# Optimization experiments

Hardware: AMD Instinct MI355X
Metric: run time of the kernel (lower is better)

The kernel has to match this reference:

```python
import jax, jax.numpy as jnp
import numpy as np

B, T, D = 2, 2048, 2048
N, K, H = 8, 4, 256
WINDOW = 1024
BASE_FREQ = 10000
ROPE_PROP = 1.0
SCALE_FACTOR = 1.0
K_MASK = -2.3819763e+38


def apply_rope(inputs, positions, base_frequency, scale_factor=1.0, rope_proportion=1.0):
    # inputs: [B,L,N,H], positions: [B,L]
    head_dim = inputs.shape[-1]
    rope_angles = int(rope_proportion * head_dim // 2)
    nope_angles = head_dim // 2 - rope_angles
    freq_exponents = 2.0 / head_dim * jnp.arange(rope_angles, dtype=jnp.float32)
    timescale = jnp.pad(base_frequency ** freq_exponents, (0, nope_angles),
                        mode='constant', constant_values=(0, jnp.inf))
    sinusoid = positions[..., None].astype(jnp.float32) / timescale[None, None, :]
    sinusoid = sinusoid[..., None, :] / scale_factor  # [B,L,1,H//2]
    sin = jnp.sin(sinusoid)
    cos = jnp.cos(sinusoid)
    first, second = jnp.split(inputs, 2, axis=-1)
    out = jnp.concatenate([first * cos - second * sin,
                           second * cos + first * sin], axis=-1)
    return out.astype(inputs.dtype)


def rms_norm(x, scale, eps=1e-6):
    var = jnp.mean(jnp.square(x.astype(jnp.float32)), axis=-1, keepdims=True)
    normed = x * jax.lax.rsqrt(var + eps)
    return (normed * (1.0 + scale)).astype(x.dtype)


def setup_inputs() -> dict:
    key = jax.random.key(0)
    ks = jax.random.split(key, 5)
    std = 0.02
    return {
        'x': jax.random.normal(ks[0], (B, T, D), jnp.float32),
        'positions': jnp.broadcast_to(jnp.arange(T, dtype=jnp.int32), (B, T)),
        'q_w': jax.random.normal(ks[1], (N, D, H), jnp.float32) * std,
        'k_w': jax.random.normal(ks[2], (K, D, H), jnp.float32) * std,
        'v_w': jax.random.normal(ks[3], (K, D, H), jnp.float32) * std,
        'o_w': jax.random.normal(ks[4], (N, H, D), jnp.float32) * std,
        'q_norm_scale': jnp.zeros((H,), jnp.float32),
        'k_norm_scale': jnp.zeros((H,), jnp.float32),
    }


def reference(x, positions, q_w, k_w, v_w, o_w, q_norm_scale, k_norm_scale):
    # QKV projections (Einsum modules)
    q = jnp.einsum('btd,ndh->btnh', x, q_w)   # [B,T,N,H]
    k = jnp.einsum('bsd,kdh->bskh', x, k_w)   # [B,S,K,H]
    v = jnp.einsum('bsd,kdh->bskh', x, v_w)
    # QK RMSNorm (gemma-style, zero-centered scale)
    q = rms_norm(q, q_norm_scale)
    k = rms_norm(k, k_norm_scale)
    # RoPE (local attention: base 10000, full proportion)
    q = apply_rope(q, positions, BASE_FREQ, SCALE_FACTOR, ROPE_PROP)
    k = apply_rope(k, positions, BASE_FREQ, SCALE_FACTOR, ROPE_PROP)
    q = q * (H ** -0.5)
    # GQA: group queries over kv heads
    G = N // K
    qg = q.reshape(B, T, K, G, H)
    logits = jnp.einsum('btkgh,bskh->btkgs', qg, k)  # [B,T,K,G,S]
    # causal + sliding-window mask from positions
    qp = positions[:, :, None]
    kp = positions[:, None, :]
    mask = (kp <= qp) & (kp > qp - WINDOW)           # [B,T,S]
    logits = jnp.where(mask[:, :, None, None, :], logits, K_MASK)
    probs = jax.nn.softmax(logits.astype(jnp.float32), axis=-1).astype(logits.dtype)
    out = jnp.einsum('btkgs,bskh->btkgh', probs, v).reshape(B, T, N, H)
    return jnp.einsum('btnh,nhd->btd', out, o_w)
```

## Files before the change

### kernel.cpp

```cpp
#include <hip/hip_runtime.h>
#include <cmath>

#define T_SEQ 2048
#define WINDOW 1024

typedef __attribute__((ext_vector_type(8))) short bf16x8;
typedef __attribute__((ext_vector_type(4))) float f32x4;
typedef __attribute__((ext_vector_type(16))) float f32x16;

__device__ __forceinline__ unsigned short f2bf(float f) {
  union { float f; unsigned int u; } v; v.f = f;
  unsigned int r = v.u + 0x7FFFu + ((v.u >> 16) & 1u);
  return (unsigned short)(r >> 16);
}
__device__ __forceinline__ float bf2f(unsigned short u) {
  union { unsigned int i; float f; } v; v.i = ((unsigned int)u) << 16;
  return v.f;
}

#define GLD16(gp, lp)                                                  \
  __builtin_amdgcn_global_load_lds(                                    \
      (__attribute__((address_space(1))) unsigned int*)(gp),           \
      (__attribute__((address_space(3))) unsigned int*)(lp), 16, 0, 0)

// ... 28 lines not shown
      tile[ty + 16 * p][tx * 4 + 0] = v.x; tile[ty + 16 * p][tx * 4 + 1] = v.y;
      tile[ty + 16 * p][tx * 4 + 2] = v.z; tile[ty + 16 * p][tx * 4 + 3] = v.w;
    }
    __syncthreads();
#pragma unroll
    for (int p = 0; p < 4; ++p) {
      int hh = ty + 16 * p;
      ushort4 o;
      o.x = f2bf(tile[tx * 4 + 0][hh]); o.y = f2bf(tile[tx * 4 + 1][hh]);
      o.z = f2bf(tile[tx * 4 + 2][hh]); o.w = f2bf(tile[tx * 4 + 3][hh]);
      *(ushort4*)&wqkvt[(size_t)(c0 + hh) * 2048 + d0 + tx * 4] = o;
    }
  } else {
    int idx = blk - 10240;
    int j0 = (idx & 31) * 64, d0 = (idx >> 5) * 64;
#pragma unroll
    for (int p = 0; p < 4; ++p) {
      float4 v = *(const float4*)&ow[(size_t)(j0 + ty + 16 * p) * 2048 + d0 + tx * 4];
      tile[ty + 16 * p][tx * 4 + 0] = v.x; tile[ty + 16 * p][tx * 4 + 1] = v.y;
      tile[ty + 16 * p][tx * 4 + 2] = v.z; tile[ty + 16 * p][tx * 4 + 3] = v.w;
    }
    __syncthreads();
#pragma unroll
    for (int p = 0; p < 4; ++p) {
      int hh = ty + 16 * p;
      ushort4 o;
      o.x = f2bf(tile[tx * 4 + 0][hh]); o.y = f2bf(tile[tx * 4 + 1][hh]);
      o.z = f2bf(tile[tx * 4 + 2][hh]); o.w = f2bf(tile[tx * 4 + 3][hh]);
      *(ushort4*)&wot[(size_t)(d0 + hh) * 2048 + j0 + tx * 4] = o;
    }
  }
}

__global__ __launch_bounds__(512) void gemm_qkv_256(
    const unsigned short* __restrict__ xb, const unsigned short* __restrict__ wt,
    unsigned short* __restrict__ qo, unsigned short* __restrict__ ko,
    unsigned short* __restrict__ vo) {
  __shared__ unsigned short lds[65536];
  const int tid = threadIdx.x;
  const int wave = tid >> 6, lane = tid & 63;
  const int wr = wave >> 2, wc = wave & 3;
  const int fm = lane & 15, fk = lane >> 4;

  const int bid = blockIdx.x;
  const int swz = (bid & 7) * 32 + (bid >> 3);
  const int m0 = (swz >> 4) * 256, n0 = (swz & 15) * 256;

  const int soff = fm * 32 + ((fk ^ ((fm >> 2) & 3)) << 3);
  const int aoff = wr * 4096 + soff;
  const int boff = wc * 2048 + soff;

  const unsigned short* Ab = xb + (size_t)m0 * 2048;
  const unsigned short* Bb = wt + (size_t)n0 * 2048;

  const int l0 = tid, l1 = tid + 512;
  const int r0 = l0 >> 2, o0 = l0 & 3;
  const int r1 = l1 >> 2, o1 = l1 & 3;
  const int sA0 = r0 * 2048 + ((o0 ^ ((r0 >> 2) & 3)) << 3);
  const int sA1 = r1 * 2048 + ((o1 ^ ((r1 >> 2) & 3)) << 3);

#define STAGE(srcbase, kofs, dstbase)                  \
  do {                                                 \
    GLD16((srcbase) + sA0 + (kofs), (dstbase) + l0 * 8); \
    GLD16((srcbase) + sA1 + (kofs), (dstbase) + l1 * 8); \
  } while (0)

  f32x4 acc[8][4];
#pragma unroll
  for (int i = 0; i < 8; ++i)
#pragma unroll
    for (int j = 0; j < 4; ++j) acc[i][j] = {0.f, 0.f, 0.f, 0.f};

  STAGE(Ab, 0,  lds + 0);
  STAGE(Bb, 0,  lds + 16384);
  STAGE(Ab, 32, lds + 8192);
  STAGE(Bb, 32, lds + 24576);
  STAGE(Ab, 64, lds + 32768);
  STAGE(Bb, 64, lds + 49152);
  asm volatile("s_waitcnt vmcnt(8)" ::: "memory");
  __builtin_amdgcn_s_barrier();

  for (int t = 0; t < 32; ++t) {
    const int p = t & 1;
    unsigned short* base = lds + p * 32768;
    unsigned short* xbase = lds + (p ^ 1) * 32768;
    const int t1 = (t < 31) ? t + 1 : 31;
    const int t2 = (t < 30) ? t + 2 : 31;

    bf16x8 a[4], b[4];
#pragma unroll
    for (int i = 0; i < 4; ++i) a[i] = *(const bf16x8*)(base + aoff + i * 512);
#pragma unroll
    for (int j = 0; j < 4; ++j) b[j] = *(const bf16x8*)(base + 16384 + boff + j * 512);
    STAGE(Ab, t1 * 64 + 32, xbase + 8192);
    __builtin_amdgcn_s_barrier();
    asm volatile("s_waitcnt lgkmcnt(0)" ::: "memory");
    __builtin_amdgcn_sched_barrier(0);
    __builtin_amdgcn_s_setprio(1);
#pragma unroll
    for (int i = 0; i < 4; ++i)
#pragma unroll
      for (int j = 0; j < 4; ++j)
        acc[i][j] = __builtin_amdgcn_mfma_f32_16x16x32_bf16(a[i], b[j], acc[i][j], 0, 0, 0);
    __builtin_amdgcn_s_setprio(0);
    __builtin_amdgcn_s_barrier();

#pragma unroll
    for (int i = 0; i < 4; ++i) a[i] = *(const bf16x8*)(base + aoff + (i + 4) * 512);
    STAGE(Bb, t1 * 64 + 32, xbase + 24576);
    __builtin_amdgcn_s_barrier();
    asm volatile("s_waitcnt lgkmcnt(0)" ::: "memory");
    __builtin_amdgcn_sched_barrier(0);
    __builtin_amdgcn_s_setprio(1);
#pragma unroll
    for (int i = 0; i < 4; ++i)
#pragma unroll
      for (int j = 0; j < 4; ++j)
        acc[i + 4][j] = __builtin_amdgcn_mfma_f32_16x16x32_bf16(a[i], b[j], acc[i + 4][j], 0, 0, 0);
    __builtin_amdgcn_s_setprio(0);
    asm volatile("s_waitcnt vmcnt(8)" ::: "memory");
    __builtin_amdgcn_s_barrier();

#pragma unroll
    for (int i = 0; i < 4; ++i) a[i] = *(const bf16x8*)(base + 8192 + aoff + i * 512);
#pragma unroll
    for (int j = 0; j < 4; ++j) b[j] = *(const bf16x8*)(base + 24576 + boff + j * 512);
    STAGE(Ab, t2 * 64, base + 0);
    __builtin_amdgcn_s_barrier();
    asm volatile("s_waitcnt lgkmcnt(0)" ::: "memory");
    __builtin_amdgcn_sched_barrier(0);
    __builtin_amdgcn_s_setprio(1);
#pragma unroll
    for (int i = 0; i < 4; ++i)
#pragma unroll
      for (int j = 0; j < 4; ++j)
        acc[i][j] = __builtin_amdgcn_mfma_f32_16x16x32_bf16(a[i], b[j], acc[i][j], 0, 0, 0);
    __builtin_amdgcn_s_setprio(0);
    __builtin_amdgcn_s_barrier();

#pragma unroll
    for (int i = 0; i < 4; ++i) a[i] = *(const bf16x8*)(base + 8192 + aoff + (i + 4) * 512);
    STAGE(Bb, t2 * 64, base + 16384);
    __builtin_amdgcn_s_barrier();
    asm volatile("s_waitcnt lgkmcnt(0)" ::: "memory");
    __builtin_amdgcn_sched_barrier(0);
    __builtin_amdgcn_s_setprio(1);
#pragma unroll
    for (int i = 0; i < 4; ++i)
#pragma unroll
      for (int j = 0; j < 4; ++j)
        acc[i + 4][j] = __builtin_amdgcn_mfma_f32_16x16x32_bf16(a[i], b[j], acc[i + 4][j], 0, 0, 0);
    __builtin_amdgcn_s_setprio(0);
    asm volatile("s_waitcnt vmcnt(8)" ::: "memory");
    __builtin_amdgcn_s_barrier();
  }
#undef STAGE

  unsigned short* obase; int ldo, cb;
  if (n0 < 2048) { obase = qo; ldo = 2048; cb = n0; }
  else if (n0 < 3072) { obase = ko; ldo = 1024; cb = n0 - 2048; }
  else { obase = vo; ldo = 1024; cb = n0 - 3072; }
  const int rbase = m0 + wr * 128 + (lane >> 4) * 4;
  const int cbase = cb + wc * 64 + fm;
#pragma unroll
  for (int i = 0; i < 8; ++i)
#pragma unroll
    for (int j = 0; j < 4; ++j)
#pragma unroll
      for (int r = 0; r < 4; ++r)
        obase[(size_t)(rbase + i * 16 + r) * ldo + cbase + j * 16] = f2bf(acc[i][j][r]);
}

__device__ __forceinline__ void gemm128_core(
    const unsigned short* __restrict__ A, const unsigned short* __restrict__ Bt,
    unsigned short* As, unsigned short* Bs, int m0, int n0, int K,
    f32x4 acc[4][4]) {
  const int tid = threadIdx.x;
  const int wave = tid >> 6, lane = tid & 63;
  const int wm = (wave & 1) << 6, wn = (wave >> 1) << 6;
  const int i0 = wave * 2, i1 = wave * 2 + 1;
  const int sr = lane >> 2;
  const int sc = (lane & 3) * 8;
  const size_t ar0 = (size_t)(m0 + i0 * 16 + sr) * K + sc;
  const size_t ar1 = (size_t)(m0 + i1 * 16 + sr) * K + sc;
  const size_t br0 = (size_t)(n0 + i0 * 16 + sr) * K + sc;
  const size_t br1 = (size_t)(n0 + i1 * 16 + sr) * K + sc;
  const int fm = lane & 15, fk = (lane >> 4) * 8;

  for (int kt = 0; kt < K; kt += 32) {
    GLD16(A + ar0 + kt, As + i0 * 512);
    GLD16(A + ar1 + kt, As + i1 * 512);
    GLD16(Bt + br0 + kt, Bs + i0 * 512);
    GLD16(Bt + br1 + kt, Bs + i1 * 512);
    __syncthreads();
    bf16x8 af[4], bv[4];
#pragma unroll
    for (int i = 0; i < 4; ++i)
      af[i] = *(const bf16x8*)&As[(wm + i * 16 + fm) * 32 + fk];
#pragma unroll
    for (int j = 0; j < 4; ++j)
      bv[j] = *(const bf16x8*)&Bs[(wn + j * 16 + fm) * 32 + fk];
#pragma unroll
    for (int i = 0; i < 4; ++i)
#pragma unroll
      for (int j = 0; j < 4; ++j)
        acc[i][j] = __builtin_amdgcn_mfma_f32_16x16x32_bf16(af[i], bv[j], acc[i][j], 0, 0, 0);
    __syncthreads();
  }
}

__global__ __launch_bounds__(256) void gemm_out_bf16(
    const unsigned short* __restrict__ ab, const unsigned short* __restrict__ wot,
    float* __restrict__ out) {
  __shared__ unsigned short As[128 * 32];
  __shared__ unsigned short Bs[128 * 32];
  const int n0 = blockIdx.x * 128, m0 = blockIdx.y * 128;
  f32x4 acc[4][4];
#pragma unroll
  for (int i = 0; i < 4; ++i)
#pragma unroll
    for (int j = 0; j < 4; ++j) acc[i][j] = {0.f, 0.f, 0.f, 0.f};
  gemm128_core(ab, wot, As, Bs, m0, n0, 2048, acc);

  const int lane = threadIdx.x & 63, wave = threadIdx.x >> 6;
  const int wm = (wave & 1) << 6, wn = (wave >> 1) << 6;
  const int rbase = m0 + wm + (lane >> 4) * 4;
  const int cbase = n0 + wn + (lane & 15);
#pragma unroll
  for (int i = 0; i < 4; ++i)
#pragma unroll
    for (int j = 0; j < 4; ++j)
#pragma unroll
      for (int r = 0; r < 4; ++r)
        out[(size_t)(rbase + i * 16 + r) * 2048 + cbase + j * 16] = acc[i][j][r];
}

__global__ __launch_bounds__(256) void postproc(
    unsigned short* __restrict__ qb, const unsigned short* __restrict__ kb,
    unsigned short* __restrict__ kpan,
    const unsigned short* __restrict__ vbf, unsigned short* __restrict__ vpan,
    const int* __restrict__ positions,
    const float* __restrict__ qns, const float* __restrict__ kns) {
  const int blk = blockIdx.x;
  const int tid = threadIdx.x;
  if (blk < 12288) {
    int row = blk * 4 + (tid >> 6);
    int lane = tid & 63;
    const unsigned short* src; const float* ns; float extra; int bt;
    bool isq = row < 32768;
    if (isq) {
      src = qb + (size_t)row * 256; ns = qns; extra = 0.0625f; bt = row >> 3;
    } else {
      int r = row - 32768;
      src = kb + (size_t)r * 256; ns = kns; extra = 1.0f; bt = r >> 2;
    }
    int pos = positions[bt];

    ushort4 u = *(const ushort4*)&src[lane << 2];
    float xv[4] = {bf2f(u.x), bf2f(u.y), bf2f(u.z), bf2f(u.w)};
    float ss = xv[0]*xv[0] + xv[1]*xv[1] + xv[2]*xv[2] + xv[3]*xv[3];
#pragma unroll
    for (int off = 1; off < 64; off <<= 1) ss += __shfl_xor(ss, off, 64);
    float rinv = rsqrtf(ss * (1.0f / 256.0f) + 1e-6f);

    float4 sc4 = *(const float4*)&ns[lane << 2];
    xv[0] *= rinv * (1.0f + sc4.x);
    xv[1] *= rinv * (1.0f + sc4.y);
    xv[2] *= rinv * (1.0f + sc4.z);
    xv[3] *= rinv * (1.0f + sc4.w);

    float ov[4];
#pragma unroll
    for (int c = 0; c < 4; ++c) ov[c] = __shfl_xor(xv[c], 32, 64);

    int hr = (lane & 31) << 2;
    float sgn = (lane < 32) ? -1.0f : 1.0f;
    ushort4 w4;
    unsigned short res[4];
#pragma unroll
    for (int c = 0; c < 4; ++c) {
      float invts = exp2f(-(float)(hr + c) * 0.10381025296523007f);
      float angle = (float)pos * invts;
      float sn, cs;
      __sincosf(angle, &sn, &cs);
      res[c] = f2bf((xv[c] * cs + sgn * ov[c] * sn) * extra);
    }
    w4.x = res[0]; w4.y = res[1]; w4.z = res[2]; w4.w = res[3];
    if (isq) {
      *(ushort4*)&qb[(size_t)row * 256 + (lane << 2)] = w4;
    } else {
      int r = row - 32768;
      int kvh = r & 3;
      int b_ = bt >> 11, t = bt & 2047;
      unsigned short* pan = kpan + (((size_t)(b_ * 4 + kvh) * 64 + (t >> 5)) * 8192);
      int s = t & 31;
      int c = lane >> 1;
      size_t el = (size_t)s * 256 + (size_t)((c ^ s) & 31) * 8 + (lane & 1) * 4;
      *(ushort4*)&pan[el] = w4;
    }
    return;
  }
  __shared__ unsigned short tile[64][68];
  int idx = blk - 12288;
  int h0 = (idx & 3) * 64;
  int t0 = ((idx >> 2) & 31) * 64;
  int z = idx >> 7;
  int tx = tid & 15, ty = tid >> 4;
  const unsigned short* src = vbf + ((size_t)(z >> 2) * 8192 + (z & 3)) * 256;
#pragma unroll
  for (int p = 0; p < 4; ++p) {
    ushort4 v = *(const ushort4*)&src[(size_t)(t0 + ty + 16 * p) * 1024 + h0 + tx * 4];
    tile[ty + 16 * p][tx * 4 + 0] = v.x; tile[ty + 16 * p][tx * 4 + 1] = v.y;
    tile[ty + 16 * p][tx * 4 + 2] = v.z; tile[ty + 16 * p][tx * 4 + 3] = v.w;
  }
  __syncthreads();
#pragma unroll
  for (int p = 0; p < 4; ++p) {
    int hh = ty + 16 * p;
    int h = h0 + hh;
    int t = t0 + tx * 4;
    int pp = t >> 5, s = t & 31;
    ushort4 o;
    o.x = tile[tx * 4 + 0][hh]; o.y = tile[tx * 4 + 1][hh];
    o.z = tile[tx * 4 + 2][hh]; o.w = tile[tx * 4 + 3][hh];
    size_t el = ((size_t)z * 64 + pp) * 8192 + (size_t)h * 32 +
                (size_t)(((s >> 3) ^ (h & 3)) & 3) * 8 + (s & 7);
    *(ushort4*)&vpan[el] = o;
  }
}

__global__ __launch_bounds__(128) void attn_mfma(
    const unsigned short* __restrict__ qb,
    const unsigned short* __restrict__ kpan,
    const unsigned short* __restrict__ vpan,
    unsigned short* __restrict__ ob) {
  __shared__ __align__(16) unsigned short Kl[8192];
  __shared__ __align__(16) unsigned short Vl[8192];
  __shared__ __align__(16) unsigned short Ps[3072];

  const int tid = threadIdx.x;
  const int w = tid >> 6, lane = tid & 63;
  const int l5 = lane >> 5, l31 = lane & 31;
  const int pair = blockIdx.x & 7;
  const int t0 = (blockIdx.x >> 3) * 32;
  const int kvh = pair >> 1, b = pair & 1;
  const int n = 2 * kvh + w;
  const int tmin = t0, tmax = t0 + 31;

  bf16x8 aq[16];
  {
    const unsigned short* qrow =
        qb + (((size_t)b * 2048 + tmin + l31) * 8 + n) * 256 + l5 * 8;
#pragma unroll
    for (int kc = 0; kc < 16; ++kc) aq[kc] = *(const bf16x8*)(qrow + kc * 16);
  }

  f32x16 O[8], lsum;
#pragma unroll
  for (int i = 0; i < 8; ++i)
#pragma unroll
    for (int r = 0; r < 16; ++r) O[i][r] = 0.f;
#pragma unroll
  for (int r = 0; r < 16; ++r) lsum[r] = 0.f;

  bf16x8 ones;
#pragma unroll
  for (int i = 0; i < 8; ++i) ones[i] = (short)0x3F80;

  const unsigned short* kpb = kpan + (size_t)(b * 4 + kvh) * 64 * 8192;
  const unsigned short* vpb = vpan + (size_t)(b * 4 + kvh) * 64 * 8192;

  int s_lo = t0 - 1024; if (s_lo < 0) s_lo = 0;
  const int s_end = t0 + 32;

  for (int s0 = s_lo; s0 < s_end; s0 += 32) {
    __syncthreads();
    const unsigned short* kp = kpb + (size_t)(s0 >> 5) * 8192;
    const unsigned short* vp = vpb + (size_t)(s0 >> 5) * 8192;
#pragma unroll
    for (int j = 0; j < 8; ++j) {
      int g = j * 128 + tid;
      GLD16(kp + g * 8, Kl + g * 8);
    }
#pragma unroll
    for (int j = 0; j < 8; ++j) {
      int g = j * 128 + tid;
      GLD16(vp + g * 8, Vl + g * 8);
    }
    __syncthreads();

    f32x16 pa, pb;
#pragma unroll
    for (int r = 0; r < 16; ++r) { pa[r] = 0.f; pb[r] = 0.f; }
#pragma unroll
    for (int kc = 0; kc < 16; kc += 2) {
      bf16x8 b0 = *(const bf16x8*)&Kl[l31 * 256 + (((kc * 2 + l5) ^ l31) & 31) * 8];
      bf16x8 b1 = *(const bf16x8*)&Kl[l31 * 256 + ((((kc + 1) * 2 + l5) ^ l31) & 31) * 8];
      pa = __builtin_amdgcn_mfma_f32_32x32x16_bf16(aq[kc], b0, pa, 0, 0, 0);
      pb = __builtin_amdgcn_mfma_f32_32x32x16_bf16(aq[kc + 1], b1, pb, 0, 0, 0);
    }

    bool allvalid = (s0 + 31 <= tmin) && (s0 >= tmax - 1023);
    int scol = s0 + l31;
#pragma unroll
    for (int r = 0; r < 16; ++r) {
      float sv = pa[r] + pb[r];
      float p = exp2f(sv * 1.442695040888963f);
      int m = (r & 3) + 8 * (r >> 2) + 4 * l5;
      if (!allvalid) {
        int dt = (tmin + m) - scol;
        p = (dt >= 0 && dt < 1024) ? p : 0.f;
      }
      Ps[w * 1536 + (l31 >> 4) * 768 + m * 24 + (l31 & 15)] = f2bf(p);
    }

    bf16x8 pf0 = *(const bf16x8*)&Ps[w * 1536 + l31 * 24 + l5 * 8];
    bf16x8 pf1 = *(const bf16x8*)&Ps[w * 1536 + 768 + l31 * 24 + l5 * 8];
    lsum = __builtin_amdgcn_mfma_f32_32x32x16_bf16(pf0, ones, lsum, 0, 0, 0);
    lsum = __builtin_amdgcn_mfma_f32_32x32x16_bf16(pf1, ones, lsum, 0, 0, 0);
#pragma unroll
    for (int hb = 0; hb < 8; ++hb) {
      int row = hb * 32 + l31;
      bf16x8 v0 = *(const bf16x8*)&Vl[row * 32 + ((l5 ^ row) & 3) * 8];
      bf16x8 v1 = *(const bf16x8*)&Vl[row * 32 + (((2 + l5) ^ row) & 3) * 8];
      O[hb] = __builtin_amdgcn_mfma_f32_32x32x16_bf16(pf0, v0, O[hb], 0, 0, 0);
      O[hb] = __builtin_amdgcn_mfma_f32_32x32x16_bf16(pf1, v1, O[hb], 0, 0, 0);
    }
  }

  unsigned short* obase = ob + (((size_t)b * 2048 + tmin) * 8 + n) * 256;
#pragma unroll
  for (int r = 0; r < 16; ++r) {
    int m = (r & 3) + 8 * (r >> 2) + 4 * l5;
    float rinv = 1.0f / lsum[r];
    size_t rowoff = (size_t)m * 2048;
#pragma unroll
    for (int hb = 0; hb < 8; ++hb)
      obase[rowoff + hb * 32 + l31] = f2bf(O[hb][r] * rinv);
  }
}

extern "C" void kernel_launch(void* const* d_in, const int* in_sizes, int n_in,
                              void* d_out, int out_size, void* d_ws, size_t ws_size,
                              hipStream_t stream) {
  const float* x   = (const float*)d_in[0];
  const int* pos   = (const int*)d_in[1];
  const float* q_w = (const float*)d_in[2];
  const float* k_w = (const float*)d_in[3];
  const float* v_w = (const float*)d_in[4];
  const float* o_w = (const float*)d_in[5];
  const float* qns = (const float*)d_in[6];
  const float* kns = (const float*)d_in[7];
  float* out = (float*)d_out;

  unsigned short* W = (unsigned short*)d_ws;
  unsigned short* qb0   = W;
  unsigned short* kb0   = W + 8388608;
  unsigned short* vbf   = W + 12582912;
  unsigned short* vpan  = W + 16777216;
  unsigned short* kpan  = W + 20971520;
  unsigned short* xb    = W + 25165824;
  unsigned short* wqkvt = W + 33554432;
  unsigned short* abuf  = wqkvt;
  unsigned short* wot   = W + 41943040;

  prep<<<dim3(11264), 256, 0, stream>>>(x, q_w, k_w, v_w, o_w, xb, wqkvt, wot);
  gemm_qkv_256<<<dim3(256), 512, 0, stream>>>(xb, wqkvt, qb0, kb0, vbf);
  postproc<<<dim3(13312), 256, 0, stream>>>(qb0, kb0, kpan, vbf, vpan, pos, qns, kns);
  attn_mfma<<<dim3(512), 128, 0, stream>>>(qb0, kpan, vpan, abuf);
  gemm_out_bf16<<<dim3(16, 32), 256, 0, stream>>>(abuf, wot, out);
}
```

Measured before the change: 345.4 us.

## Double-buffer K/V tiles in attention and widen blocks to two query tiles

The attention kernel now runs 256 threads per block covering 64 query rows (two 32-row tiles times two heads), so each K/V tile loaded to LDS is shared by twice as many waves. K/V loads are double-buffered: the next tile is prefetched with async global-to-LDS loads while the current one is computed, using explicit vmcnt waits and barriers. Waves skip tiles outside their own window. The V panel swizzle also changes to a different XOR pattern to reduce LDS bank conflicts. In exchange the grid halves to 256 blocks, LDS use roughly doubles, and waves idle at barriers on tiles outside their window.

```diff
diff --git a/kernel.cpp b/kernel.cpp
--- a/kernel.cpp
+++ b/kernel.cpp
@@ -376,28 +376,28 @@
     o.x = tile[tx * 4 + 0][hh]; o.y = tile[tx * 4 + 1][hh];
     o.z = tile[tx * 4 + 2][hh]; o.w = tile[tx * 4 + 3][hh];
     size_t el = ((size_t)z * 64 + pp) * 8192 + (size_t)h * 32 +
-                (size_t)(((s >> 3) ^ (h & 3)) & 3) * 8 + (s & 7);
+                (size_t)(((s >> 3) ^ h ^ (h >> 2)) & 3) * 8 + (s & 7);
     *(ushort4*)&vpan[el] = o;
   }
 }
 
-__global__ __launch_bounds__(128) void attn_mfma(
+__global__ __launch_bounds__(256) void attn_mfma(
     const unsigned short* __restrict__ qb,
     const unsigned short* __restrict__ kpan,
     const unsigned short* __restrict__ vpan,
     unsigned short* __restrict__ ob) {
-  __shared__ __align__(16) unsigned short Kl[8192];
-  __shared__ __align__(16) unsigned short Vl[8192];
-  __shared__ __align__(16) unsigned short Ps[3072];
+  __shared__ __align__(16) unsigned short Kl[2][8192];
+  __shared__ __align__(16) unsigned short Vl[2][8192];
+  __shared__ __align__(16) unsigned short Ps[6144];
 
   const int tid = threadIdx.x;
   const int w = tid >> 6, lane = tid & 63;
   const int l5 = lane >> 5, l31 = lane & 31;
   const int pair = blockIdx.x & 7;
-  const int t0 = (blockIdx.x >> 3) * 32;
+  const int t0 = (blockIdx.x >> 3) * 64;
   const int kvh = pair >> 1, b = pair & 1;
-  const int n = 2 * kvh + w;
-  const int tmin = t0, tmax = t0 + 31;
+  const int n = 2 * kvh + (w & 1);
+  const int tmin = t0 + (w >> 1) * 32, tmax = tmin + 31;
 
   bf16x8 aq[16];
   {
@@ -423,61 +423,80 @@
   const unsigned short* vpb = vpan + (size_t)(b * 4 + kvh) * 64 * 8192;
 
   int s_lo = t0 - 1024; if (s_lo < 0) s_lo = 0;
-  const int s_end = t0 + 32;
-
-  for (int s0 = s_lo; s0 < s_end; s0 += 32) {
-    __syncthreads();
-    const unsigned short* kp = kpb + (size_t)(s0 >> 5) * 8192;
-    const unsigned short* vp = vpb + (size_t)(s0 >> 5) * 8192;
-#pragma unroll
-    for (int j = 0; j < 8; ++j) {
-      int g = j * 128 + tid;
-      GLD16(kp + g * 8, Kl + g * 8);
-    }
-#pragma unroll
-    for (int j = 0; j < 8; ++j) {
-      int g = j * 128 + tid;
-      GLD16(vp + g * 8, Vl + g * 8);
-    }
-    __syncthreads();
-
-    f32x16 pa, pb;
-#pragma unroll
-    for (int r = 0; r < 16; ++r) { pa[r] = 0.f; pb[r] = 0.f; }
-#pragma unroll
-    for (int kc = 0; kc < 16; kc += 2) {
-      bf16x8 b0 = *(const bf16x8*)&Kl[l31 * 256 + (((kc * 2 + l5) ^ l31) & 31) * 8];
-      bf16x8 b1 = *(const bf16x8*)&Kl[l31 * 256 + ((((kc + 1) * 2 + l5) ^ l31) & 31) * 8];
-      pa = __builtin_amdgcn_mfma_f32_32x32x16_bf16(aq[kc], b0, pa, 0, 0, 0);
-      pb = __builtin_amdgcn_mfma_f32_32x32x16_bf16(aq[kc + 1], b1, pb, 0, 0, 0);
-    }
-
-    bool allvalid = (s0 + 31 <= tmin) && (s0 >= tmax - 1023);
-    int scol = s0 + l31;
-#pragma unroll
-    for (int r = 0; r < 16; ++r) {
-      float sv = pa[r] + pb[r];
-      float p = exp2f(sv * 1.442695040888963f);
-      int m = (r & 3) + 8 * (r >> 2) + 4 * l5;
-      if (!allvalid) {
-        int dt = (tmin + m) - scol;
-        p = (dt >= 0 && dt < 1024) ? p : 0.f;
+  const int nt = ((t0 + 64) - s_lo) >> 5;
+
+  {
+    const unsigned short* kp = kpb + (size_t)(s_lo >> 5) * 8192;
+    const unsigned short* vp = vpb + (size_t)(s_lo >> 5) * 8192;
+#pragma unroll
+    for (int j = 0; j < 4; ++j) { int g = (j * 256 + tid) * 8; GLD16(kp + g, &Kl[0][g]); }
+#pragma unroll
+    for (int j = 0; j < 4; ++j) { int g = (j * 256 + tid) * 8; GLD16(vp + g, &Vl[0][g]); }
+  }
+
+  for (int it = 0; it < nt; ++it) {
+    const int cur = it & 1;
+    const int s0 = s_lo + it * 32;
+    if (it + 1 < nt) {
+      const unsigned short* kp = kpb + ((size_t)(s0 >> 5) + 1) * 8192;
+      const unsigned short* vp = vpb + ((size_t)(s0 >> 5) + 1) * 8192;
+#pragma unroll
+      for (int j = 0; j < 4; ++j) { int g = (j * 256 + tid) * 8; GLD16(kp + g, &Kl[cur ^ 1][g]); }
+#pragma unroll
+      for (int j = 0; j < 4; ++j) { int g = (j * 256 + tid) * 8; GLD16(vp + g, &Vl[cur ^ 1][g]); }
+      asm volatile("s_waitcnt vmcnt(8)" ::: "memory");
+    } else {
+      asm volatile("s_waitcnt vmcnt(0)" ::: "memory");
+    }
+    __builtin_amdgcn_s_barrier();
+    __builtin_amdgcn_sched_barrier(0);
+
+    if ((s0 <= tmax) && (s0 + 31 >= tmin - 1023)) {
+      const unsigned short* Kc = Kl[cur];
+      const unsigned short* Vc = Vl[cur];
+
+      f32x16 pa, pb;
+#pragma unroll
+      for (int r = 0; r < 16; ++r) { pa[r] = 0.f; pb[r] = 0.f; }
+#pragma unroll
+      for (int kc = 0; kc < 16; kc += 2) {
+        bf16x8 b0 = *(const bf16x8*)&Kc[l31 * 256 + (((kc * 2 + l5) ^ l31) & 31) * 8];
+        bf16x8 b1 = *(const bf16x8*)&Kc[l31 * 256 + ((((kc + 1) * 2 + l5) ^ l31) & 31) * 8];
+        pa = __builtin_amdgcn_mfma_f32_32x32x16_bf16(aq[kc], b0, pa, 0, 0, 0);
+        pb = __builtin_amdgcn_mfma_f32_32x32x16_bf16(aq[kc + 1], b1, pb, 0, 0, 0);
       }
-      Ps[w * 1536 + (l31 >> 4) * 768 + m * 24 + (l31 & 15)] = f2bf(p);
-    }
-
-    bf16x8 pf0 = *(const bf16x8*)&Ps[w * 1536 + l31 * 24 + l5 * 8];
-    bf16x8 pf1 = *(const bf16x8*)&Ps[w * 1536 + 768 + l31 * 24 + l5 * 8];
-    lsum = __builtin_amdgcn_mfma_f32_32x32x16_bf16(pf0, ones, lsum, 0, 0, 0);
-    lsum = __builtin_amdgcn_mfma_f32_32x32x16_bf16(pf1, ones, lsum, 0, 0, 0);
-#pragma unroll
-    for (int hb = 0; hb < 8; ++hb) {
-      int row = hb * 32 + l31;
-      bf16x8 v0 = *(const bf16x8*)&Vl[row * 32 + ((l5 ^ row) & 3) * 8];
-      bf16x8 v1 = *(const bf16x8*)&Vl[row * 32 + (((2 + l5) ^ row) & 3) * 8];
-      O[hb] = __builtin_amdgcn_mfma_f32_32x32x16_bf16(pf0, v0, O[hb], 0, 0, 0);
-      O[hb] = __builtin_amdgcn_mfma_f32_32x32x16_bf16(pf1, v1, O[hb], 0, 0, 0);
-    }
+
+      bool allvalid = (s0 + 31 <= tmin) && (s0 >= tmax - 1023);
+      int scol = s0 + l31;
+#pragma unroll
+      for (int r = 0; r < 16; ++r) {
+        float sv = pa[r] + pb[r];
+        float p = exp2f(sv * 1.442695040888963f);
+        int m = (r & 3) + 8 * (r >> 2) + 4 * l5;
+        if (!allvalid) {
+          int dt = (tmin + m) - scol;
+          p = (dt >= 0 && dt < 1024) ? p : 0.f;
+        }
+        Ps[w * 1536 + (l31 >> 4) * 768 + m * 24 + (l31 & 15)] = f2bf(p);
+      }
+
+      bf16x8 pf0 = *(const bf16x8*)&Ps[w * 1536 + l31 * 24 + l5 * 8];
+      bf16x8 pf1 = *(const bf16x8*)&Ps[w * 1536 + 768 + l31 * 24 + l5 * 8];
+      lsum = __builtin_amdgcn_mfma_f32_32x32x16_bf16(pf0, ones, lsum, 0, 0, 0);
+      lsum = __builtin_amdgcn_mfma_f32_32x32x16_bf16(pf1, ones, lsum, 0, 0, 0);
+#pragma unroll
+      for (int hb = 0; hb < 8; ++hb) {
+        int row = hb * 32 + l31;
+        int gh = (row ^ (row >> 2)) & 3;
+        bf16x8 v0 = *(const bf16x8*)&Vc[row * 32 + ((l5 ^ gh) & 3) * 8];
+        bf16x8 v1 = *(const bf16x8*)&Vc[row * 32 + (((2 + l5) ^ gh) & 3) * 8];
+        O[hb] = __builtin_amdgcn_mfma_f32_32x32x16_bf16(pf0, v0, O[hb], 0, 0, 0);
+        O[hb] = __builtin_amdgcn_mfma_f32_32x32x16_bf16(pf1, v1, O[hb], 0, 0, 0);
+      }
+    }
+    asm volatile("s_waitcnt lgkmcnt(0)" ::: "memory");
+    __builtin_amdgcn_sched_barrier(0);
+    __builtin_amdgcn_s_barrier();
   }
 
   unsigned short* obase = ob + (((size_t)b * 2048 + tmin) * 8 + n) * 256;
@@ -519,6 +538,6 @@
   prep<<<dim3(11264), 256, 0, stream>>>(x, q_w, k_w, v_w, o_w, xb, wqkvt, wot);
   gemm_qkv_256<<<dim3(256), 512, 0, stream>>>(xb, wqkvt, qb0, kb0, vbf);
   postproc<<<dim3(13312), 256, 0, stream>>>(qb0, kb0, kpan, vbf, vpan, pos, qns, kns);
-  attn_mfma<<<dim3(512), 128, 0, stream>>>(qb0, kpan, vpan, abuf);
+  attn_mfma<<<dim3(256), 256, 0, stream>>>(qb0, kpan, vpan, abuf);
   gemm_out_bf16<<<dim3(16, 32), 256, 0, stream>>>(abuf, wot, out);
 }
```

Measured after the change: 357.4 us. +3.5%, slower.

## Load K/V panels directly into registers with double-buffered K in attention

Applied to the files above, without the earlier changes.

The attention kernel now runs one wave per block and reads K and V panels straight from global memory into MFMA-operand registers, dropping the shared-memory staging and block barriers. The postproc kernel rewrites the K and V panel layouts so each lane's fragment is a contiguous 16-byte load. K tiles are prefetched one iteration ahead through a ping-pong register buffer, and V loads are split around the softmax. This trades LDS traffic and syncs for higher register pressure and duplicated global/L2 reads, since the two heads sharing a KV head no longer share a staged tile.

```diff
diff --git a/kernel.cpp b/kernel.cpp
--- a/kernel.cpp
+++ b/kernel.cpp
@@ -346,8 +346,7 @@
       int b_ = bt >> 11, t = bt & 2047;
       unsigned short* pan = kpan + (((size_t)(b_ * 4 + kvh) * 64 + (t >> 5)) * 8192);
       int s = t & 31;
-      int c = lane >> 1;
-      size_t el = (size_t)s * 256 + (size_t)((c ^ s) & 31) * 8 + (lane & 1) * 4;
+      size_t el = (size_t)(lane >> 1) * 256 + (size_t)s * 8 + (lane & 1) * 4;
       *(ushort4*)&pan[el] = w4;
     }
     return;
@@ -375,28 +374,29 @@
     ushort4 o;
     o.x = tile[tx * 4 + 0][hh]; o.y = tile[tx * 4 + 1][hh];
     o.z = tile[tx * 4 + 2][hh]; o.w = tile[tx * 4 + 3][hh];
-    size_t el = ((size_t)z * 64 + pp) * 8192 + (size_t)h * 32 +
-                (size_t)(((s >> 3) ^ (h & 3)) & 3) * 8 + (s & 7);
+    size_t el = ((size_t)z * 64 + pp) * 8192 + (size_t)(h >> 5) * 1024 +
+                (size_t)((s >> 3) & 3) * 256 + (size_t)(h & 31) * 8 + (s & 7);
     *(ushort4*)&vpan[el] = o;
   }
 }
 
-__global__ __launch_bounds__(128) void attn_mfma(
+__global__ __launch_bounds__(64, 1) void attn_mfma(
     const unsigned short* __restrict__ qb,
     const unsigned short* __restrict__ kpan,
     const unsigned short* __restrict__ vpan,
     unsigned short* __restrict__ ob) {
-  __shared__ __align__(16) unsigned short Kl[8192];
-  __shared__ __align__(16) unsigned short Vl[8192];
-  __shared__ __align__(16) unsigned short Ps[3072];
-
-  const int tid = threadIdx.x;
-  const int w = tid >> 6, lane = tid & 63;
+  __shared__ __align__(16) unsigned short Ps[1536];
+
+  const int lane = threadIdx.x & 63;
   const int l5 = lane >> 5, l31 = lane & 31;
-  const int pair = blockIdx.x & 7;
-  const int t0 = (blockIdx.x >> 3) * 32;
+  const int blk = blockIdx.x;
+  const int pair = blk & 7;
+  const int r = blk >> 3;
+  const int tt = r & 63;
+  const int head = r >> 6;
   const int kvh = pair >> 1, b = pair & 1;
-  const int n = 2 * kvh + w;
+  const int n = 2 * kvh + head;
+  const int t0 = tt * 32;
   const int tmin = t0, tmax = t0 + 31;
 
   bf16x8 aq[16];
@@ -411,9 +411,9 @@
 #pragma unroll
   for (int i = 0; i < 8; ++i)
 #pragma unroll
-    for (int r = 0; r < 16; ++r) O[i][r] = 0.f;
-#pragma unroll
-  for (int r = 0; r < 16; ++r) lsum[r] = 0.f;
+    for (int rr = 0; rr < 16; ++rr) O[i][rr] = 0.f;
+#pragma unroll
+  for (int rr = 0; rr < 16; ++rr) lsum[rr] = 0.f;
 
   bf16x8 ones;
 #pragma unroll
@@ -423,72 +423,96 @@
   const unsigned short* vpb = vpan + (size_t)(b * 4 + kvh) * 64 * 8192;
 
   int s_lo = t0 - 1024; if (s_lo < 0) s_lo = 0;
-  const int s_end = t0 + 32;
-
-  for (int s0 = s_lo; s0 < s_end; s0 += 32) {
-    __syncthreads();
-    const unsigned short* kp = kpb + (size_t)(s0 >> 5) * 8192;
-    const unsigned short* vp = vpb + (size_t)(s0 >> 5) * 8192;
-#pragma unroll
-    for (int j = 0; j < 8; ++j) {
-      int g = j * 128 + tid;
-      GLD16(kp + g * 8, Kl + g * 8);
-    }
-#pragma unroll
-    for (int j = 0; j < 8; ++j) {
-      int g = j * 128 + tid;
-      GLD16(vp + g * 8, Vl + g * 8);
-    }
-    __syncthreads();
-
-    f32x16 pa, pb;
-#pragma unroll
-    for (int r = 0; r < 16; ++r) { pa[r] = 0.f; pb[r] = 0.f; }
-#pragma unroll
-    for (int kc = 0; kc < 16; kc += 2) {
-      bf16x8 b0 = *(const bf16x8*)&Kl[l31 * 256 + (((kc * 2 + l5) ^ l31) & 31) * 8];
-      bf16x8 b1 = *(const bf16x8*)&Kl[l31 * 256 + ((((kc + 1) * 2 + l5) ^ l31) & 31) * 8];
-      pa = __builtin_amdgcn_mfma_f32_32x32x16_bf16(aq[kc], b0, pa, 0, 0, 0);
-      pb = __builtin_amdgcn_mfma_f32_32x32x16_bf16(aq[kc + 1], b1, pb, 0, 0, 0);
-    }
-
-    bool allvalid = (s0 + 31 <= tmin) && (s0 >= tmax - 1023);
-    int scol = s0 + l31;
-#pragma unroll
-    for (int r = 0; r < 16; ++r) {
-      float sv = pa[r] + pb[r];
-      float p = exp2f(sv * 1.442695040888963f);
-      int m = (r & 3) + 8 * (r >> 2) + 4 * l5;
-      if (!allvalid) {
-        int dt = (tmin + m) - scol;
-        p = (dt >= 0 && dt < 1024) ? p : 0.f;
-      }
-      Ps[w * 1536 + (l31 >> 4) * 768 + m * 24 + (l31 & 15)] = f2bf(p);
-    }
-
-    bf16x8 pf0 = *(const bf16x8*)&Ps[w * 1536 + l31 * 24 + l5 * 8];
-    bf16x8 pf1 = *(const bf16x8*)&Ps[w * 1536 + 768 + l31 * 24 + l5 * 8];
-    lsum = __builtin_amdgcn_mfma_f32_32x32x16_bf16(pf0, ones, lsum, 0, 0, 0);
-    lsum = __builtin_amdgcn_mfma_f32_32x32x16_bf16(pf1, ones, lsum, 0, 0, 0);
-#pragma unroll
-    for (int hb = 0; hb < 8; ++hb) {
-      int row = hb * 32 + l31;
-      bf16x8 v0 = *(const bf16x8*)&Vl[row * 32 + ((l5 ^ row) & 3) * 8];
-      bf16x8 v1 = *(const bf16x8*)&Vl[row * 32 + (((2 + l5) ^ row) & 3) * 8];
-      O[hb] = __builtin_amdgcn_mfma_f32_32x32x16_bf16(pf0, v0, O[hb], 0, 0, 0);
-      O[hb] = __builtin_amdgcn_mfma_f32_32x32x16_bf16(pf1, v1, O[hb], 0, 0, 0);
-    }
-  }
+  const int p0 = s_lo >> 5;
+  const int nt = ((t0 + 32) - s_lo) >> 5;
+
+  const int koff = l5 * 256 + l31 * 8;
+  const int voff0 = l5 * 256 + l31 * 8;
+  const int voff1 = (2 + l5) * 256 + l31 * 8;
+
+  bf16x8 KA[16], KB[16];
+
+  {
+    const unsigned short* kp = kpb + (size_t)p0 * 8192;
+#pragma unroll
+    for (int u = 0; u < 16; ++u) KA[u] = *(const bf16x8*)(kp + u * 512 + koff);
+  }
+
+#define ATTN_BODY(CUR, NXT)                                                   \
+  do {                                                                        \
+    const int s0 = s_lo + it * 32;                                            \
+    if (it + 1 < nt) {                  \
+      const unsigned short* kp = kpb + (size_t)(p0 + it + 1) * 8192;          \
+      _Pragma("unroll")                                                       \
+      for (int u = 0; u < 16; ++u) NXT[u] = *(const bf16x8*)(kp + u * 512 + koff); \
+    }                                                                         \
+    const unsigned short* vp = vpb + (size_t)(p0 + it) * 8192;                \
+    bf16x8 Vv0[8], Vv1[8];                                                    \
+    _Pragma("unroll")         \
+    for (int hb = 0; hb < 4; ++hb) {                                          \
+      Vv0[hb * 2]     = *(const bf16x8*)(vp + hb * 1024 + voff0);             \
+      Vv0[hb * 2 + 1] = *(const bf16x8*)(vp + hb * 1024 + voff1);             \
+    }                                                                         \
+    f32x16 pa, pb;                                                            \
+    _Pragma("unroll")                                                         \
+    for (int rr = 0; rr < 16; ++rr) { pa[rr] = 0.f; pb[rr] = 0.f; }           \
+    _Pragma("unroll")                                                         \
+    for (int kc = 0; kc < 16; kc += 2) {                                      \
+      pa = __builtin_amdgcn_mfma_f32_32x32x16_bf16(aq[kc], CUR[kc], pa, 0, 0, 0); \
+      pb = __builtin_amdgcn_mfma_f32_32x32x16_bf16(aq[kc + 1], CUR[kc + 1], pb, 0, 0, 0); \
+    }                                                                         \
+    bool allvalid = (s0 + 31 <= tmin) && (s0 >= tmax - 1023);                 \
+    int scol = s0 + l31;                                                      \
+    _Pragma("unroll")                                                         \
+    for (int rr = 0; rr < 16; ++rr) {                                         \
+      float sv = pa[rr] + pb[rr];                                             \
+      float p = exp2f(sv * 1.442695040888963f);                               \
+      int m = (rr & 3) + 8 * (rr >> 2) + 4 * l5;                              \
+      if (!allvalid) {                                                        \
+        int dt = (tmin + m) - scol;                                           \
+        p = (dt >= 0 && dt < 1024) ? p : 0.f;                                 \
+      }                                                                       \
+      Ps[(l31 >> 4) * 768 + m * 24 + (l31 & 15)] = f2bf(p);                   \
+    }                                                                         \
+    _Pragma("unroll") \
+    for (int hb = 4; hb < 8; ++hb) {                                          \
+      Vv1[(hb - 4) * 2]     = *(const bf16x8*)(vp + hb * 1024 + voff0);       \
+      Vv1[(hb - 4) * 2 + 1] = *(const bf16x8*)(vp + hb * 1024 + voff1);       \
+    }                                                                         \
+    bf16x8 pf0 = *(const bf16x8*)&Ps[l31 * 24 + l5 * 8];                      \
+    bf16x8 pf1 = *(const bf16x8*)&Ps[768 + l31 * 24 + l5 * 8];                \
+    lsum = __builtin_amdgcn_mfma_f32_32x32x16_bf16(pf0, ones, lsum, 0, 0, 0); \
+    lsum = __builtin_amdgcn_mfma_f32_32x32x16_bf16(pf1, ones, lsum, 0, 0, 0); \
+    _Pragma("unroll")                                                         \
+    for (int hb = 0; hb < 4; ++hb) {                                          \
+      O[hb] = __builtin_amdgcn_mfma_f32_32x32x16_bf16(pf0, Vv0[hb * 2], O[hb], 0, 0, 0); \
+      O[hb] = __builtin_amdgcn_mfma_f32_32x32x16_bf16(pf1, Vv0[hb * 2 + 1], O[hb], 0, 0, 0); \
+    }                                                                         \
+    _Pragma("unroll")                                                         \
+    for (int hb = 4; hb < 8; ++hb) {                                          \
+      O[hb] = __builtin_amdgcn_mfma_f32_32x32x16_bf16(pf0, Vv1[(hb - 4) * 2], O[hb], 0, 0, 0); \
+      O[hb] = __builtin_amdgcn_mfma_f32_32x32x16_bf16(pf1, Vv1[(hb - 4) * 2 + 1], O[hb], 0, 0, 0); \
+    }                                                                         \
+  } while (0)
+
+  int it = 0;
+  while (true) {
+    ATTN_BODY(KA, KB);
+    if (++it == nt) break;
+    ATTN_BODY(KB, KA);
+    if (++it == nt) break;
+  }
+#undef ATTN_BODY
 
   unsigned short* obase = ob + (((size_t)b * 2048 + tmin) * 8 + n) * 256;
 #pragma unroll
-  for (int r = 0; r < 16; ++r) {
-    int m = (r & 3) + 8 * (r >> 2) + 4 * l5;
-    float rinv = 1.0f / lsum[r];
+  for (int rr = 0; rr < 16; ++rr) {
+    int m = (rr & 3) + 8 * (rr >> 2) + 4 * l5;
+    float rinv = 1.0f / lsum[rr];
     size_t rowoff = (size_t)m * 2048;
 #pragma unroll
     for (int hb = 0; hb < 8; ++hb)
-      obase[rowoff + hb * 32 + l31] = f2bf(O[hb][r] * rinv);
+      obase[rowoff + hb * 32 + l31] = f2bf(O[hb][rr] * rinv);
   }
 }
 
@@ -519,6 +543,6 @@
   prep<<<dim3(11264), 256, 0, stream>>>(x, q_w, k_w, v_w, o_w, xb, wqkvt, wot);
   gemm_qkv_256<<<dim3(256), 512, 0, stream>>>(xb, wqkvt, qb0, kb0, vbf);
   postproc<<<dim3(13312), 256, 0, stream>>>(qb0, kb0, kpan, vbf, vpan, pos, qns, kns);
-  attn_mfma<<<dim3(512), 128, 0, stream>>>(qb0, kpan, vpan, abuf);
+  attn_mfma<<<dim3(1024), 64, 0, stream>>>(qb0, kpan, vpan, abuf);
   gemm_out_bf16<<<dim3(16, 32), 256, 0, stream>>>(abuf, wot, out);
 }
```

New measurement: 532.9 us. +54.3%, slower.

## Reuse pipelined 256x256 GEMM core for output projection and reswizzle V panel

Applied to the files above, without the earlier changes.

Moves the software-pipelined 256x256 MFMA GEMM loop into a shared device function and uses it for the output projection as well, in place of the simple 128x128 single-buffered GEMM. The new kernel launches 128 blocks of 512 threads with a grouped block swizzle, aiming for more operand reuse and load/compute overlap. Separately, the V panel layout and the matching LDS read swizzle in attention now XOR in h>>2 to reduce LDS bank conflicts. The trade-off is that only 128 large blocks cover the GPU for the output GEMM, fewer than the number of CUs, which could leave some units idle.

```diff
diff --git a/kernel.cpp b/kernel.cpp
--- a/kernel.cpp
+++ b/kernel.cpp
@@ -84,6 +84,109 @@
   }
 }
 
+__device__ __forceinline__ void gemm256_core(
+    const unsigned short* __restrict__ Ab, const unsigned short* __restrict__ Bb,
+    unsigned short* lds, f32x4 acc[8][4], int aoff, int boff) {
+  const int tid = threadIdx.x;
+
+  const int l0 = tid, l1 = tid + 512;
+  const int r0 = l0 >> 2, o0 = l0 & 3;
+  const int r1 = l1 >> 2, o1 = l1 & 3;
+  const int sA0 = r0 * 2048 + ((o0 ^ ((r0 >> 2) & 3)) << 3);
+  const int sA1 = r1 * 2048 + ((o1 ^ ((r1 >> 2) & 3)) << 3);
+
+#define STAGE(srcbase, kofs, dstbase)                  \
+  do {                                                 \
+    GLD16((srcbase) + sA0 + (kofs), (dstbase) + l0 * 8); \
+    GLD16((srcbase) + sA1 + (kofs), (dstbase) + l1 * 8); \
+  } while (0)
+
+  STAGE(Ab, 0,  lds + 0);
+  STAGE(Bb, 0,  lds + 16384);
+  STAGE(Ab, 32, lds + 8192);
+  STAGE(Bb, 32, lds + 24576);
+  STAGE(Ab, 64, lds + 32768);
+  STAGE(Bb, 64, lds + 49152);
+  asm volatile("s_waitcnt vmcnt(8)" ::: "memory");
+  __builtin_amdgcn_s_barrier();
+
+  for (int t = 0; t < 32; ++t) {
+    const int p = t & 1;
+    unsigned short* base = lds + p * 32768;
+    unsigned short* xbase = lds + (p ^ 1) * 32768;
+    const int t1 = (t < 31) ? t + 1 : 31;
+    const int t2 = (t < 30) ? t + 2 : 31;
+
+    bf16x8 a[4], b[4];
+#pragma unroll
+    for (int i = 0; i < 4; ++i) a[i] = *(const bf16x8*)(base + aoff + i * 512);
+#pragma unroll
+    for (int j = 0; j < 4; ++j) b[j] = *(const bf16x8*)(base + 16384 + boff + j * 512);
+    STAGE(Ab, t1 * 64 + 32, xbase + 8192);
+    __builtin_amdgcn_s_barrier();
+    asm volatile("s_waitcnt lgkmcnt(0)" ::: "memory");
+    __builtin_amdgcn_sched_barrier(0);
+    __builtin_amdgcn_s_setprio(1);
+#pragma unroll
+    for (int i = 0; i < 4; ++i)
+#pragma unroll
+      for (int j = 0; j < 4; ++j)
+        acc[i][j] = __builtin_amdgcn_mfma_f32_16x16x32_bf16(a[i], b[j], acc[i][j], 0, 0, 0);
+    __builtin_amdgcn_s_setprio(0);
+    __builtin_amdgcn_s_barrier();
+
+#pragma unroll
+    for (int i = 0; i < 4; ++i) a[i] = *(const bf16x8*)(base + aoff + (i + 4) * 512);
+    STAGE(Bb, t1 * 64 + 32, xbase + 24576);
+    __builtin_amdgcn_s_barrier();
+    asm volatile("s_waitcnt lgkmcnt(0)" ::: "memory");
+    __builtin_amdgcn_sched_barrier(0);
+    __builtin_amdgcn_s_setprio(1);
+#pragma unroll
+    for (int i = 0; i < 4; ++i)
+#pragma unroll
+      for (int j = 0; j < 4; ++j)
+        acc[i + 4][j] = __builtin_amdgcn_mfma_f32_16x16x32_bf16(a[i], b[j], acc[i + 4][j], 0, 0, 0);
+    __builtin_amdgcn_s_setprio(0);
+    asm volatile("s_waitcnt vmcnt(8)" ::: "memory");
+    __builtin_amdgcn_s_barrier();
+
+#pragma unroll
+    for (int i = 0; i < 4; ++i) a[i] = *(const bf16x8*)(base + 8192 + aoff + i * 512);
+#pragma unroll
+    for (int j = 0; j < 4; ++j) b[j] = *(const bf16x8*)(base + 24576 + boff + j * 512);
+    STAGE(Ab, t2 * 64, base + 0);
+    __builtin_amdgcn_s_barrier();
+    asm volatile("s_waitcnt lgkmcnt(0)" ::: "memory");
+    __builtin_amdgcn_sched_barrier(0);
+    __builtin_amdgcn_s_setprio(1);
+#pragma unroll
+    for (int i = 0; i < 4; ++i)
+#pragma unroll
+      for (int j = 0; j < 4; ++j)
+        acc[i][j] = __builtin_amdgcn_mfma_f32_16x16x32_bf16(a[i], b[j], acc[i][j], 0, 0, 0);
+    __builtin_amdgcn_s_setprio(0);
+    __builtin_amdgcn_s_barrier();
+
+#pragma unroll
+    for (int i = 0; i < 4; ++i) a[i] = *(const bf16x8*)(base + 8192 + aoff + (i + 4) * 512);
+    STAGE(Bb, t2 * 64, base + 16384);
+    __builtin_amdgcn_s_barrier();
+    asm volatile("s_waitcnt lgkmcnt(0)" ::: "memory");
+    __builtin_amdgcn_sched_barrier(0);
+    __builtin_amdgcn_s_setprio(1);
+#pragma unroll
+    for (int i = 0; i < 4; ++i)
+#pragma unroll
+      for (int j = 0; j < 4; ++j)
+        acc[i + 4][j] = __builtin_amdgcn_mfma_f32_16x16x32_bf16(a[i], b[j], acc[i + 4][j], 0, 0, 0);
+    __builtin_amdgcn_s_setprio(0);
+    asm volatile("s_waitcnt vmcnt(8)" ::: "memory");
+    __builtin_amdgcn_s_barrier();
+  }
+#undef STAGE
+}
+
 __global__ __launch_bounds__(512) void gemm_qkv_256(
     const unsigned short* __restrict__ xb, const unsigned short* __restrict__ wt,
     unsigned short* __restrict__ qo, unsigned short* __restrict__ ko,
@@ -102,111 +205,13 @@
   const int aoff = wr * 4096 + soff;
   const int boff = wc * 2048 + soff;
 
-  const unsigned short* Ab = xb + (size_t)m0 * 2048;
-  const unsigned short* Bb = wt + (size_t)n0 * 2048;
-
-  const int l0 = tid, l1 = tid + 512;
-  const int r0 = l0 >> 2, o0 = l0 & 3;
-  const int r1 = l1 >> 2, o1 = l1 & 3;
-  const int sA0 = r0 * 2048 + ((o0 ^ ((r0 >> 2) & 3)) << 3);
-  const int sA1 = r1 * 2048 + ((o1 ^ ((r1 >> 2) & 3)) << 3);
-
-#define STAGE(srcbase, kofs, dstbase)                  \
-  do {                                                 \
-    GLD16((srcbase) + sA0 + (kofs), (dstbase) + l0 * 8); \
-    GLD16((srcbase) + sA1 + (kofs), (dstbase) + l1 * 8); \
-  } while (0)
-
   f32x4 acc[8][4];
 #pragma unroll
   for (int i = 0; i < 8; ++i)
 #pragma unroll
     for (int j = 0; j < 4; ++j) acc[i][j] = {0.f, 0.f, 0.f, 0.f};
 
-  STAGE(Ab, 0,  lds + 0);
-  STAGE(Bb, 0,  lds + 16384);
-  STAGE(Ab, 32, lds + 8192);
-  STAGE(Bb, 32, lds + 24576);
-  STAGE(Ab, 64, lds + 32768);
-  STAGE(Bb, 64, lds + 49152);
-  asm volatile("s_waitcnt vmcnt(8)" ::: "memory");
-  __builtin_amdgcn_s_barrier();
-
-  for (int t = 0; t < 32; ++t) {
-    const int p = t & 1;
-    unsigned short* base = lds + p * 32768;
-    unsigned short* xbase = lds + (p ^ 1) * 32768;
-    const int t1 = (t < 31) ? t + 1 : 31;
-    const int t2 = (t < 30) ? t + 2 : 31;
-
-    bf16x8 a[4], b[4];
-#pragma unroll
-    for (int i = 0; i < 4; ++i) a[i] = *(const bf16x8*)(base + aoff + i * 512);
-#pragma unroll
-    for (int j = 0; j < 4; ++j) b[j] = *(const bf16x8*)(base + 16384 + boff + j * 512);
-    STAGE(Ab, t1 * 64 + 32, xbase + 8192);
-    __builtin_amdgcn_s_barrier();
-    asm volatile("s_waitcnt lgkmcnt(0)" ::: "memory");
-    __builtin_amdgcn_sched_barrier(0);
-    __builtin_amdgcn_s_setprio(1);
-#pragma unroll
-    for (int i = 0; i < 4; ++i)
-#pragma unroll
-      for (int j = 0; j < 4; ++j)
-        acc[i][j] = __builtin_amdgcn_mfma_f32_16x16x32_bf16(a[i], b[j], acc[i][j], 0, 0, 0);
-    __builtin_amdgcn_s_setprio(0);
-    __builtin_amdgcn_s_barrier();
-
-#pragma unroll
-    for (int i = 0; i < 4; ++i) a[i] = *(const bf16x8*)(base + aoff + (i + 4) * 512);
-    STAGE(Bb, t1 * 64 + 32, xbase + 24576);
-    __builtin_amdgcn_s_barrier();
-    asm volatile("s_waitcnt lgkmcnt(0)" ::: "memory");
-    __builtin_amdgcn_sched_barrier(0);
-    __builtin_amdgcn_s_setprio(1);
-#pragma unroll
-    for (int i = 0; i < 4; ++i)
-#pragma unroll
-      for (int j = 0; j < 4; ++j)
-        acc[i + 4][j] = __builtin_amdgcn_mfma_f32_16x16x32_bf16(a[i], b[j], acc[i + 4][j], 0, 0, 0);
-    __builtin_amdgcn_s_setprio(0);
-    asm volatile("s_waitcnt vmcnt(8)" ::: "memory");
-    __builtin_amdgcn_s_barrier();
-
-#pragma unroll
-    for (int i = 0; i < 4; ++i) a[i] = *(const bf16x8*)(base + 8192 + aoff + i * 512);
-#pragma unroll
-    for (int j = 0; j < 4; ++j) b[j] = *(const bf16x8*)(base + 24576 + boff + j * 512);
-    STAGE(Ab, t2 * 64, base + 0);
-    __builtin_amdgcn_s_barrier();
-    asm volatile("s_waitcnt lgkmcnt(0)" ::: "memory");
-    __builtin_amdgcn_sched_barrier(0);
-    __builtin_amdgcn_s_setprio(1);
-#pragma unroll
-    for (int i = 0; i < 4; ++i)
-#pragma unroll
-      for (int j = 0; j < 4; ++j)
-        acc[i][j] = __builtin_amdgcn_mfma_f32_16x16x32_bf16(a[i], b[j], acc[i][j], 0, 0, 0);
-    __builtin_amdgcn_s_setprio(0);
-    __builtin_amdgcn_s_barrier();
-
-#pragma unroll
-    for (int i = 0; i < 4; ++i) a[i] = *(const bf16x8*)(base + 8192 + aoff + (i + 4) * 512);
-    STAGE(Bb, t2 * 64, base + 16384);
-    __builtin_amdgcn_s_barrier();
-    asm volatile("s_waitcnt lgkmcnt(0)" ::: "memory");
-    __builtin_amdgcn_sched_barrier(0);
-    __builtin_amdgcn_s_setprio(1);
-#pragma unroll
-    for (int i = 0; i < 4; ++i)
-#pragma unroll
-      for (int j = 0; j < 4; ++j)
-        acc[i + 4][j] = __builtin_amdgcn_mfma_f32_16x16x32_bf16(a[i], b[j], acc[i + 4][j], 0, 0, 0);
-    __builtin_amdgcn_s_setprio(0);
-    asm volatile("s_waitcnt vmcnt(8)" ::: "memory");
-    __builtin_amdgcn_s_barrier();
-  }
-#undef STAGE
+  gemm256_core(xb + (size_t)m0 * 2048, wt + (size_t)n0 * 2048, lds, acc, aoff, boff);
 
   unsigned short* obase; int ldo, cb;
   if (n0 < 2048) { obase = qo; ldo = 2048; cb = n0; }
@@ -223,63 +228,35 @@
         obase[(size_t)(rbase + i * 16 + r) * ldo + cbase + j * 16] = f2bf(acc[i][j][r]);
 }
 
-__device__ __forceinline__ void gemm128_core(
-    const unsigned short* __restrict__ A, const unsigned short* __restrict__ Bt,
-    unsigned short* As, unsigned short* Bs, int m0, int n0, int K,
-    f32x4 acc[4][4]) {
+__global__ __launch_bounds__(512) void gemm_out_256(
+    const unsigned short* __restrict__ ab, const unsigned short* __restrict__ wot,
+    float* __restrict__ out) {
+  __shared__ unsigned short lds[65536];
   const int tid = threadIdx.x;
   const int wave = tid >> 6, lane = tid & 63;
-  const int wm = (wave & 1) << 6, wn = (wave >> 1) << 6;
-  const int i0 = wave * 2, i1 = wave * 2 + 1;
-  const int sr = lane >> 2;
-  const int sc = (lane & 3) * 8;
-  const size_t ar0 = (size_t)(m0 + i0 * 16 + sr) * K + sc;
-  const size_t ar1 = (size_t)(m0 + i1 * 16 + sr) * K + sc;
-  const size_t br0 = (size_t)(n0 + i0 * 16 + sr) * K + sc;
-  const size_t br1 = (size_t)(n0 + i1 * 16 + sr) * K + sc;
-  const int fm = lane & 15, fk = (lane >> 4) * 8;
-
-  for (int kt = 0; kt < K; kt += 32) {
-    GLD16(A + ar0 + kt, As + i0 * 512);
-    GLD16(A + ar1 + kt, As + i1 * 512);
-    GLD16(Bt + br0 + kt, Bs + i0 * 512);
-    GLD16(Bt + br1 + kt, Bs + i1 * 512);
-    __syncthreads();
-    bf16x8 af[4], bv[4];
-#pragma unroll
-    for (int i = 0; i < 4; ++i)
-      af[i] = *(const bf16x8*)&As[(wm + i * 16 + fm) * 32 + fk];
-#pragma unroll
-    for (int j = 0; j < 4; ++j)
-      bv[j] = *(const bf16x8*)&Bs[(wn + j * 16 + fm) * 32 + fk];
-#pragma unroll
-    for (int i = 0; i < 4; ++i)
-#pragma unroll
-      for (int j = 0; j < 4; ++j)
-        acc[i][j] = __builtin_amdgcn_mfma_f32_16x16x32_bf16(af[i], bv[j], acc[i][j], 0, 0, 0);
-    __syncthreads();
-  }
-}
-
-__global__ __launch_bounds__(256) void gemm_out_bf16(
-    const unsigned short* __restrict__ ab, const unsigned short* __restrict__ wot,
-    float* __restrict__ out) {
-  __shared__ unsigned short As[128 * 32];
-  __shared__ unsigned short Bs[128 * 32];
-  const int n0 = blockIdx.x * 128, m0 = blockIdx.y * 128;
-  f32x4 acc[4][4];
-#pragma unroll
-  for (int i = 0; i < 4; ++i)
+  const int wr = wave >> 2, wc = wave & 3;
+  const int fm = lane & 15, fk = lane >> 4;
+
+  const int bid = blockIdx.x;
+  const int swz = (bid & 7) * 16 + (bid >> 3);
+  const int m0 = (swz >> 3) * 256, n0 = (swz & 7) * 256;
+
+  const int soff = fm * 32 + ((fk ^ ((fm >> 2) & 3)) << 3);
+  const int aoff = wr * 4096 + soff;
+  const int boff = wc * 2048 + soff;
+
+  f32x4 acc[8][4];
+#pragma unroll
+  for (int i = 0; i < 8; ++i)
 #pragma unroll
     for (int j = 0; j < 4; ++j) acc[i][j] = {0.f, 0.f, 0.f, 0.f};
-  gemm128_core(ab, wot, As, Bs, m0, n0, 2048, acc);
-
-  const int lane = threadIdx.x & 63, wave = threadIdx.x >> 6;
-  const int wm = (wave & 1) << 6, wn = (wave >> 1) << 6;
-  const int rbase = m0 + wm + (lane >> 4) * 4;
-  const int cbase = n0 + wn + (lane & 15);
-#pragma unroll
-  for (int i = 0; i < 4; ++i)
+
+  gemm256_core(ab + (size_t)m0 * 2048, wot + (size_t)n0 * 2048, lds, acc, aoff, boff);
+
+  const int rbase = m0 + wr * 128 + (lane >> 4) * 4;
+  const int cbase = n0 + wc * 64 + fm;
+#pragma unroll
+  for (int i = 0; i < 8; ++i)
 #pragma unroll
     for (int j = 0; j < 4; ++j)
 #pragma unroll
@@ -376,7 +353,7 @@
     o.x = tile[tx * 4 + 0][hh]; o.y = tile[tx * 4 + 1][hh];
     o.z = tile[tx * 4 + 2][hh]; o.w = tile[tx * 4 + 3][hh];
     size_t el = ((size_t)z * 64 + pp) * 8192 + (size_t)h * 32 +
-                (size_t)(((s >> 3) ^ (h & 3)) & 3) * 8 + (s & 7);
+                (size_t)(((s >> 3) ^ h ^ (h >> 2)) & 3) * 8 + (s & 7);
     *(ushort4*)&vpan[el] = o;
   }
 }
@@ -473,8 +450,9 @@
 #pragma unroll
     for (int hb = 0; hb < 8; ++hb) {
       int row = hb * 32 + l31;
-      bf16x8 v0 = *(const bf16x8*)&Vl[row * 32 + ((l5 ^ row) & 3) * 8];
-      bf16x8 v1 = *(const bf16x8*)&Vl[row * 32 + (((2 + l5) ^ row) & 3) * 8];
+      int gh = (row ^ (row >> 2)) & 3;
+      bf16x8 v0 = *(const bf16x8*)&Vl[row * 32 + ((l5 ^ gh) & 3) * 8];
+      bf16x8 v1 = *(const bf16x8*)&Vl[row * 32 + (((2 + l5) ^ gh) & 3) * 8];
       O[hb] = __builtin_amdgcn_mfma_f32_32x32x16_bf16(pf0, v0, O[hb], 0, 0, 0);
       O[hb] = __builtin_amdgcn_mfma_f32_32x32x16_bf16(pf1, v1, O[hb], 0, 0, 0);
     }
@@ -520,5 +498,5 @@
   gemm_qkv_256<<<dim3(256), 512, 0, stream>>>(xb, wqkvt, qb0, kb0, vbf);
   postproc<<<dim3(13312), 256, 0, stream>>>(qb0, kb0, kpan, vbf, vpan, pos, qns, kns);
   attn_mfma<<<dim3(512), 128, 0, stream>>>(qb0, kpan, vpan, abuf);
-  gemm_out_bf16<<<dim3(16, 32), 256, 0, stream>>>(abuf, wot, out);
-}
+  gemm_out_256<<<dim3(128), 512, 0, stream>>>(abuf, wot, out);
+}
```

Result: no change. 346.4 us (+0.3%).
